# Kernel optimization log

Measured on AMD Instinct MI355X. Metric: run time of the kernel, lower is better.

The kernel has to match this reference:

```python
import jax, jax.numpy as jnp
import numpy as np

B = 16
NS = 1024   # coarse points per cloud
NT = 4096   # fine (skip) points per cloud
CIN = 256
CSK = 64
H = 256
K = 3


def setup_inputs() -> dict:
    key = jax.random.key(0)
    ks = jax.random.split(key, 8)
    x = jax.random.normal(ks[0], (B * NS, CIN), dtype=jnp.float32)
    pos = jax.random.normal(ks[1], (B * NS, 3), dtype=jnp.float32)
    x_skip = jax.random.normal(ks[2], (B * NT, CSK), dtype=jnp.float32)
    pos_skip = jax.random.normal(ks[3], (B * NT, 3), dtype=jnp.float32)
    batch = jnp.repeat(jnp.arange(B, dtype=jnp.int64), NS)
    batch_skip = jnp.repeat(jnp.arange(B, dtype=jnp.int64), NT)
    W1 = jax.random.normal(ks[4], (CIN + CSK, H), dtype=jnp.float32) / np.sqrt(CIN + CSK)
    b1 = jnp.zeros((H,), dtype=jnp.float32)
    W2 = jax.random.normal(ks[5], (H, H), dtype=jnp.float32) / np.sqrt(H)
    b2 = jnp.zeros((H,), dtype=jnp.float32)
    return {"x": x, "pos": pos, "x_skip": x_skip, "pos_skip": pos_skip,
            "W1": W1, "b1": b1, "W2": W2, "b2": b2,
            "batch": batch, "batch_skip": batch_skip}


def _knn_interpolate(x, pos, pos_skip):
    # x: [B*NS, C], pos: [B*NS, 3], pos_skip: [B*NT, 3]; equal-size clouds,
    # batch ids are contiguous so per-cloud kNN == reshape to [B, N, .]
    xb = x.reshape(B, NS, -1)
    pb = pos.reshape(B, NS, 3)
    qb = pos_skip.reshape(B, NT, 3)
    # squared distances [B, NT, NS]
    d2 = jnp.sum((qb[:, :, None, :] - pb[:, None, :, :]) ** 2, axis=-1)
    neg_d2k, idx = jax.lax.top_k(-d2, K)            # [B, NT, K]
    w = 1.0 / jnp.maximum(-neg_d2k, 1e-16)          # inverse squared distance
    feats = jax.vmap(lambda xc, ic: xc[ic])(xb, idx)  # [B, NT, K, C]
    y = jnp.sum(feats * w[..., None], axis=2) / jnp.sum(w, axis=2, keepdims=True)
    return y.reshape(B * NT, -1)


def reference(x, pos, x_skip, pos_skip, W1, b1, W2, b2, batch, batch_skip):
    xi = _knn_interpolate(x, pos, pos_skip)          # [B*NT, CIN]
    h = jnp.concatenate([xi, x_skip], axis=1)        # [B*NT, CIN+CSK]
    h = jax.nn.relu(h @ W1 + b1)
    h = jax.nn.relu(h @ W2 + b2)
    return (h, pos_skip, batch_skip)
```

## Files before the change

### kernel.cpp

```cpp
#include <hip/hip_runtime.h>
#include <hip/hip_bf16.h>

#define BB   16
#define NS   1024
#define NT   4096
#define CIN  256
#define CSK  64
#define HD   256
#define K1   (CIN + CSK)
#define MTOT (BB * NT)

typedef __attribute__((ext_vector_type(4))) float f32x4;
typedef __attribute__((ext_vector_type(8))) __bf16 bf16x8;
typedef __attribute__((ext_vector_type(4))) unsigned short ushort4v;

#define W1F_OFF 0u
#define W2F_OFF 163840u

static __device__ __forceinline__ unsigned short f2bf(float f) {
    union { float f; unsigned int u; } v; v.f = f;
    unsigned int r = (v.u + 0x7FFFu + ((v.u >> 16) & 1u)) >> 16;
    return (unsigned short)r;
}
static __device__ __forceinline__ unsigned short f2bf_hw(float f) {
    union { __bf16 b; unsigned short u; } v; v.b = (__bf16)f;
    return v.u;
}

#define PREP_B1 (K1 * HD / 256)
#define PREP_B2 (HD * HD / 256)
#define PREP_B3 ((MTOT * 3) / 256)
__global__ __launch_bounds__(256) void prep_kernel(
    const float* __restrict__ W1, const float* __restrict__ W2,
    const float* __restrict__ pos_skip,
    unsigned short* __restrict__ W1f, unsigned short* __restrict__ W2f,
    float* __restrict__ out)
{
    const int b = blockIdx.x;
    if (b < PREP_B1 + PREP_B2) {
        const bool is1 = b < PREP_B1;
        const int id = (is1 ? b : b - PREP_B1) * 256 + threadIdx.x;
        const int j    = id & 7;
        const int lane = (id >> 3) & 63;
        const int n    = (id >> 9) & 15;
        const int kblk = id >> 13;
        const int k   = kblk * 32 + (lane >> 4) * 8 + j;
        const int col = n * 16 + (lane & 15);
        if (is1) W1f[id] = f2bf(W1[(size_t)k * HD + col]);
        else     W2f[id] = f2bf(W2[(size_t)k * HD + col]);
    } else {
        const int i = (b - PREP_B1 - PREP_B2) * 256 + threadIdx.x;
        const size_t o1 = (size_t)MTOT * HD;
        out[o1 + i] = pos_skip[i];
        if (i < MTOT) out[o1 + (size_t)MTOT * 3 + i] = (float)(i >> 12);
    }
}

__global__ __launch_bounds__(256, 4) void fp_fused_kernel(
    const float* __restrict__ x, const float* __restrict__ x_skip,
    const float* __restrict__ pos, const float* __restrict__ pos_skip,
    const unsigned short* __restrict__ W1f, const unsigned short* __restrict__ W2f,
    const float* __restrict__ b1, const float* __restrict__ b2,
    float* __restrict__ out)
{
    __shared__ __align__(16) unsigned short ldsA[10 * 4 * 512];

    const int tid = threadIdx.x;
    const int w = tid >> 6, lane = tid & 63;
    const int l15 = lane & 15, lk = lane >> 4;

    const int bid   = blockIdx.x;
    const int xcd   = bid & 7;
    const int j     = bid >> 3;
    const int cloud = xcd + 8 * (j >> 6);
    const int bm    = cloud * 64 + (j & 63);

    int   myi0, myi1, myi2;
    float myw0, myw1, myw2;
    {
        float4* sp = (float4*)ldsA;
        const float* pc = pos + (size_t)cloud * NS * 3;
        for (int i = tid; i < NS; i += 256)
            sp[i] = make_float4(pc[i * 3 + 0], pc[i * 3 + 1], pc[i * 3 + 2], 0.f);
        __syncthreads();

        const int p  = tid & 3;
        const int rg = bm * 64 + (tid >> 2);
        const float qx = pos_skip[rg * 3 + 0];
        const float qy = pos_skip[rg * 3 + 1];
        const float qz = pos_skip[rg * 3 + 2];

        double b0 = 1e300, b1k = 1e300, b2k = 1e300;
        double si = (double)p;
        #pragma unroll 4
        for (int i = 0; i < NS / 4; ++i) {
            const int s = i * 4 + p;
            float4 c = sp[s];
            float dx = qx - c.x, dy = qy - c.y, dz = qz - c.z;
            float d = dx * dx + dy * dy + dz * dz;
            double key = fma((double)__float_as_uint(d), 1024.0, si);
            si += 4.0;
            double nb0 = fmin(b0, key);
            double nb1 = fmax(b0, fmin(b1k, key));
            double nb2 = fmax(b1k, fmin(b2k, key));
            b0 = nb0; b1k = nb1; b2k = nb2;
        }
        #pragma unroll
        for (int m = 1; m <= 2; m <<= 1) {
            double o0 = __shfl_xor(b0, m, 64);
            double o1 = __shfl_xor(b1k, m, 64);
            double o2 = __shfl_xor(b2k, m, 64);
            double nb0, nb1, nb2;
            nb0 = fmin(b0, o0); nb1 = fmax(b0, fmin(b1k, o0)); nb2 = fmax(b1k, fmin(b2k, o0));
            b0 = nb0; b1k = nb1; b2k = nb2;
            nb0 = fmin(b0, o1); nb1 = fmax(b0, fmin(b1k, o1)); nb2 = fmax(b1k, fmin(b2k, o1));
            b0 = nb0; b1k = nb1; b2k = nb2;
            nb0 = fmin(b0, o2); nb1 = fmax(b0, fmin(b1k, o2)); nb2 = fmax(b1k, fmin(b2k, o2));
            b0 = nb0; b1k = nb1; b2k = nb2;
        }
        unsigned long long k0 = (unsigned long long)b0;
        unsigned long long k1 = (unsigned long long)b1k;
        unsigned long long k2 = (unsigned long long)b2k;
        myi0 = (int)(k0 & 1023ull);
        myi1 = (int)(k1 & 1023ull);
        myi2 = (int)(k2 & 1023ull);
        float d0 = __uint_as_float((unsigned int)(k0 >> 10));
        float d1 = __uint_as_float((unsigned int)(k1 >> 10));
        float d2 = __uint_as_float((unsigned int)(k2 >> 10));
        float w0 = 1.f / fmaxf(d0, 1e-16f);
        float w1 = 1.f / fmaxf(d1, 1e-16f);
        float w2 = 1.f / fmaxf(d2, 1e-16f);
        float inv = 1.f / (w0 + w1 + w2);
        myw0 = w0 * inv; myw1 = w1 * inv; myw2 = w2 * inv;
        __syncthreads();
    }

    {
        const int cb  = cloud * NS;
        const int kbm = lane >> 3;
        const int lkm = (lane >> 1) & 3;
        const int em  = lane & 1;
        const int kbs = 8 + (lane >> 5);
        const int lks = (lane >> 3) & 3;
        const int jjs = lane & 7;
        #pragma unroll
        for (int r16 = 0; r16 < 16; ++r16) {
            const int src = r16 * 4;
            const int i0 = cb + __shfl(myi0, src, 64);
            const int i1 = cb + __shfl(myi1, src, 64);
            const int i2 = cb + __shfl(myi2, src, 64);
            const float w0 = __shfl(myw0, src, 64);
            const float w1 = __shfl(myw1, src, 64);
            const float w2 = __shfl(myw2, src, 64);
            const int row = w * 16 + r16;
            const int rg  = bm * 64 + row;
            f32x4 a = *(const f32x4*)(x + (size_t)i0 * CIN + lane * 4);
            f32x4 b = *(const f32x4*)(x + (size_t)i1 * CIN + lane * 4);
            f32x4 c = *(const f32x4*)(x + (size_t)i2 * CIN + lane * 4);
            float s = x_skip[(size_t)rg * CSK + lane];
            f32x4 r = a * w0 + b * w1 + c * w2;
            int H = ((kbm * 4 + w) * 64 + (r16 + 16 * lkm)) * 8 + 4 * em;
            H ^= (kbm & 7) << 3;
            ushort4v o4 = { f2bf_hw(r[0]), f2bf_hw(r[1]), f2bf_hw(r[2]), f2bf_hw(r[3]) };
            *(ushort4v*)&ldsA[H] = o4;
            int H2 = ((kbs * 4 + w) * 64 + (r16 + 16 * lks)) * 8 + jjs;
            H2 ^= (kbs & 7) << 3;
            ldsA[H2] = f2bf_hw(s);
        }
    }
    __syncthreads();

    const unsigned short* w1p = W1f + (w * 4) * 512 + lane * 8;
    const unsigned short* w2p = W2f + (w * 4) * 512 + lane * 8;

    f32x4 acc[4][4];
    #pragma unroll
    for (int mf = 0; mf < 4; ++mf)
        #pragma unroll
        for (int nf = 0; nf < 4; ++nf)
            acc[mf][nf] = f32x4{0.f, 0.f, 0.f, 0.f};

    {
        bf16x8 bc[4], bn[4];
        #pragma unroll
        for (int nf = 0; nf < 4; ++nf)
            bc[nf] = *(const bf16x8*)(w1p + nf * 512);
        #pragma unroll
        for (int kb = 0; kb < 10; ++kb) {
            if (kb < 9) {
                #pragma unroll
                for (int nf = 0; nf < 4; ++nf)
                    bn[nf] = *(const bf16x8*)(w1p + (size_t)(kb + 1) * 8192 + nf * 512);
            }
            bf16x8 a[4];
            #pragma unroll
            for (int mf = 0; mf < 4; ++mf) {
                int aoff = ((kb * 4 + mf) * 64 + lane) * 8;
                aoff ^= (kb & 7) << 3;
                a[mf] = *(const bf16x8*)&ldsA[aoff];
            }
            #pragma unroll
            for (int mf = 0; mf < 4; ++mf)
                #pragma unroll
                for (int nf = 0; nf < 4; ++nf)
                    acc[mf][nf] = __builtin_amdgcn_mfma_f32_16x16x32_bf16(
                        a[mf], bc[nf], acc[mf][nf], 0, 0, 0);
            #pragma unroll
            for (int nf = 0; nf < 4; ++nf) bc[nf] = bn[nf];
        }
    }
    __syncthreads();

    #pragma unroll
    for (int nf = 0; nf < 4; ++nf) {
        const int col = w * 64 + nf * 16 + l15;
        const float bv = b1[col];
        const int kb2   = 2 * w + (nf >> 1);
        const int lane2 = lk * 4 + 16 * ((nf & 1) * 2 + (l15 >> 3));
        #pragma unroll
        for (int mf = 0; mf < 4; ++mf) {
            #pragma unroll
            for (int r = 0; r < 4; ++r) {
                float v = fmaxf(acc[mf][nf][r] + bv, 0.f);
                ldsA[((kb2 * 4 + mf) * 64 + lane2 + r) * 8 + (l15 & 7)] = f2bf_hw(v);
            }
        }
    }
    __syncthreads();

    f32x4 acc2[4][4];
    #pragma unroll
    for (int mf = 0; mf < 4; ++mf)
        #pragma unroll
        for (int nf = 0; nf < 4; ++nf)
            acc2[mf][nf] = f32x4{0.f, 0.f, 0.f, 0.f};

    {
        bf16x8 bc[4], bn[4];
        #pragma unroll
        for (int nf = 0; nf < 4; ++nf)
            bc[nf] = *(const bf16x8*)(w2p + nf * 512);
        #pragma unroll
        for (int kb = 0; kb < 8; ++kb) {
            if (kb < 7) {
                #pragma unroll
                for (int nf = 0; nf < 4; ++nf)
                    bn[nf] = *(const bf16x8*)(w2p + (size_t)(kb + 1) * 8192 + nf * 512);
            }
            bf16x8 a[4];
            #pragma unroll
            for (int mf = 0; mf < 4; ++mf)
                a[mf] = *(const bf16x8*)&ldsA[((kb * 4 + mf) * 64 + lane) * 8];
            #pragma unroll
            for (int mf = 0; mf < 4; ++mf)
                #pragma unroll
                for (int nf = 0; nf < 4; ++nf)
                    acc2[mf][nf] = __builtin_amdgcn_mfma_f32_16x16x32_bf16(
                        a[mf], bc[nf], acc2[mf][nf], 0, 0, 0);
            #pragma unroll
            for (int nf = 0; nf < 4; ++nf) bc[nf] = bn[nf];
        }
    }

    const int rbase = bm * 64 + lk * 4;
    const int cbase = w * 64 + l15;
    #pragma unroll
    for (int nf = 0; nf < 4; ++nf) {
        const int col = cbase + nf * 16;
        const float bv = b2[col];
        #pragma unroll
        for (int mf = 0; mf < 4; ++mf) {
            #pragma unroll
            for (int r = 0; r < 4; ++r) {
                float v = fmaxf(acc2[mf][nf][r] + bv, 0.f);
                out[(size_t)(rbase + mf * 16 + r) * HD + col] = v;
            }
        }
    }
}

extern "C" void kernel_launch(void* const* d_in, const int* in_sizes, int n_in,
                              void* d_out, int out_size, void* d_ws, size_t ws_size,
                              hipStream_t stream)
{
    const float* x        = (const float*)d_in[0];
    const float* pos      = (const float*)d_in[1];
    const float* x_skip   = (const float*)d_in[2];
    const float* pos_skip = (const float*)d_in[3];
    const float* W1       = (const float*)d_in[4];
    const float* b1       = (const float*)d_in[5];
    const float* W2       = (const float*)d_in[6];
    const float* b2       = (const float*)d_in[7];
    float* out = (float*)d_out;

    char* ws = (char*)d_ws;
    unsigned short* W1f  = (unsigned short*)(ws + W1F_OFF);
    unsigned short* W2f  = (unsigned short*)(ws + W2F_OFF);

    prep_kernel<<<PREP_B1 + PREP_B2 + PREP_B3, 256, 0, stream>>>(
        W1, W2, pos_skip, W1f, W2f, out);
    fp_fused_kernel<<<MTOT / 64, 256, 0, stream>>>(
        x, x_skip, pos, pos_skip, W1f, W2f, b1, b2, out);
}
```

Before: 62.84 us.

## Replace packed-double top-3 kNN with float/index pairwise insertion network

The per-query top-3 search now tracks float distances and unsigned indices separately instead of packing them into double keys with fp64 min/max. Candidates are processed two at a time: the pair is sorted first and then merged into the running top-3 with a short compare network. The cross-lane reduction uses explicit tie-breaking on index. Separately, the first W1 fragment loads are issued at kernel start so their latency overlaps the kNN phase, at the cost of extra live registers during the search.

```diff
diff --git a/kernel.cpp b/kernel.cpp
--- a/kernel.cpp
+++ b/kernel.cpp
@@ -75,6 +75,13 @@
     const int cloud = xcd + 8 * (j >> 6);
     const int bm    = cloud * 64 + (j & 63);
 
+    const unsigned short* w1p = W1f + (w * 4) * 512 + lane * 8;
+    const unsigned short* w2p = W2f + (w * 4) * 512 + lane * 8;
+    bf16x8 bpre[4];
+    #pragma unroll
+    for (int nf = 0; nf < 4; ++nf)
+        bpre[nf] = *(const bf16x8*)(w1p + nf * 512);
+
     int   myi0, myi1, myi2;
     float myw0, myw1, myw2;
     {
@@ -90,46 +97,61 @@
         const float qy = pos_skip[rg * 3 + 1];
         const float qz = pos_skip[rg * 3 + 2];
 
-        double b0 = 1e300, b1k = 1e300, b2k = 1e300;
-        double si = (double)p;
-        #pragma unroll 4
-        for (int i = 0; i < NS / 4; ++i) {
-            const int s = i * 4 + p;
-            float4 c = sp[s];
-            float dx = qx - c.x, dy = qy - c.y, dz = qz - c.z;
-            float d = dx * dx + dy * dy + dz * dz;
-            double key = fma((double)__float_as_uint(d), 1024.0, si);
-            si += 4.0;
-            double nb0 = fmin(b0, key);
-            double nb1 = fmax(b0, fmin(b1k, key));
-            double nb2 = fmax(b1k, fmin(b2k, key));
-            b0 = nb0; b1k = nb1; b2k = nb2;
+        float d0 = 1e30f, d1k = 1e30f, d2k = 1e30f;
+        unsigned i0 = 0, i1 = 0, i2 = 0;
+        #pragma unroll 2
+        for (int ii = 0; ii < NS / 8; ++ii) {
+            const int slo = ii * 8 + p;
+            const int shi = slo + 4;
+            float4 ca = sp[slo];
+            float4 cb = sp[shi];
+            float dxa = qx - ca.x, dya = qy - ca.y, dza = qz - ca.z;
+            float da = dxa * dxa + dya * dya + dza * dza;
+            float dxb = qx - cb.x, dyb = qy - cb.y, dzb = qz - cb.z;
+            float db = dxb * dxb + dyb * dyb + dzb * dzb;
+            bool cs = db < da;
+            float    dlo = cs ? db : da,           dhi = cs ? da : db;
+            unsigned ilo = cs ? (unsigned)shi : (unsigned)slo;
+            unsigned ihi = cs ? (unsigned)slo : (unsigned)shi;
+            bool c0 = dlo < d0;
+            float    x0d = c0 ? dlo : d0,  x1d = c0 ? d0 : dlo;
+            unsigned x0i = c0 ? ilo : i0,  x1i = c0 ? i0 : ilo;
+            bool cy = dhi < d1k;
+            float    y0d = cy ? dhi : d1k;
+            unsigned y0i = cy ? ihi : i1;
+            bool cr = y0d < x1d;
+            float    r1d = cr ? y0d : x1d, td = cr ? x1d : y0d;
+            unsigned r1i = cr ? y0i : x1i; unsigned ti = cr ? x1i : y0i;
+            bool c2 = td < d2k;
+            float    r2d = c2 ? td : d2k;
+            unsigned r2i = c2 ? ti : i2;
+            d0 = x0d; i0 = x0i; d1k = r1d; i1 = r1i; d2k = r2d; i2 = r2i;
         }
         #pragma unroll
         for (int m = 1; m <= 2; m <<= 1) {
-            double o0 = __shfl_xor(b0, m, 64);
-            double o1 = __shfl_xor(b1k, m, 64);
-            double o2 = __shfl_xor(b2k, m, 64);
-            double nb0, nb1, nb2;
-            nb0 = fmin(b0, o0); nb1 = fmax(b0, fmin(b1k, o0)); nb2 = fmax(b1k, fmin(b2k, o0));
-            b0 = nb0; b1k = nb1; b2k = nb2;
-            nb0 = fmin(b0, o1); nb1 = fmax(b0, fmin(b1k, o1)); nb2 = fmax(b1k, fmin(b2k, o1));
-            b0 = nb0; b1k = nb1; b2k = nb2;
-            nb0 = fmin(b0, o2); nb1 = fmax(b0, fmin(b1k, o2)); nb2 = fmax(b1k, fmin(b2k, o2));
-            b0 = nb0; b1k = nb1; b2k = nb2;
-        }
-        unsigned long long k0 = (unsigned long long)b0;
-        unsigned long long k1 = (unsigned long long)b1k;
-        unsigned long long k2 = (unsigned long long)b2k;
-        myi0 = (int)(k0 & 1023ull);
-        myi1 = (int)(k1 & 1023ull);
-        myi2 = (int)(k2 & 1023ull);
-        float d0 = __uint_as_float((unsigned int)(k0 >> 10));
-        float d1 = __uint_as_float((unsigned int)(k1 >> 10));
-        float d2 = __uint_as_float((unsigned int)(k2 >> 10));
+            float    od0 = __shfl_xor(d0, m, 64);
+            float    od1 = __shfl_xor(d1k, m, 64);
+            float    od2 = __shfl_xor(d2k, m, 64);
+            unsigned oi0 = (unsigned)__shfl_xor((int)i0, m, 64);
+            unsigned oi1 = (unsigned)__shfl_xor((int)i1, m, 64);
+            unsigned oi2 = (unsigned)__shfl_xor((int)i2, m, 64);
+            float od[3] = { od0, od1, od2 };
+            unsigned oi[3] = { oi0, oi1, oi2 };
+            #pragma unroll
+            for (int e = 0; e < 3; ++e) {
+                float dd = od[e]; unsigned ss = oi[e];
+                bool lt0 = (dd < d0)  || (dd == d0  && ss < i0);
+                bool lt1 = (dd < d1k) || (dd == d1k && ss < i1);
+                bool lt2 = (dd < d2k) || (dd == d2k && ss < i2);
+                d2k = lt1 ? d1k : (lt2 ? dd : d2k);  i2 = lt1 ? i1 : (lt2 ? ss : i2);
+                d1k = lt0 ? d0  : (lt1 ? dd : d1k);  i1 = lt0 ? i0 : (lt1 ? ss : i1);
+                d0  = lt0 ? dd  : d0;                i0 = lt0 ? ss : i0;
+            }
+        }
+        myi0 = (int)i0; myi1 = (int)i1; myi2 = (int)i2;
         float w0 = 1.f / fmaxf(d0, 1e-16f);
-        float w1 = 1.f / fmaxf(d1, 1e-16f);
-        float w2 = 1.f / fmaxf(d2, 1e-16f);
+        float w1 = 1.f / fmaxf(d1k, 1e-16f);
+        float w2 = 1.f / fmaxf(d2k, 1e-16f);
         float inv = 1.f / (w0 + w1 + w2);
         myw0 = w0 * inv; myw1 = w1 * inv; myw2 = w2 * inv;
         __syncthreads();
@@ -170,9 +192,6 @@
     }
     __syncthreads();
 
-    const unsigned short* w1p = W1f + (w * 4) * 512 + lane * 8;
-    const unsigned short* w2p = W2f + (w * 4) * 512 + lane * 8;
-
     f32x4 acc[4][4];
     #pragma unroll
     for (int mf = 0; mf < 4; ++mf)
@@ -183,8 +202,7 @@
     {
         bf16x8 bc[4], bn[4];
         #pragma unroll
-        for (int nf = 0; nf < 4; ++nf)
-            bc[nf] = *(const bf16x8*)(w1p + nf * 512);
+        for (int nf = 0; nf < 4; ++nf) bc[nf] = bpre[nf];
         #pragma unroll
         for (int kb = 0; kb < 10; ++kb) {
             if (kb < 9) {
```

Result: slower. 67.79 us (+7.9%).

## Process two row tiles per block and overlap next tile's kNN with MLP MFMAs

Applied to the files above, without the earlier changes.

Each block now handles two 64-row tiles of the same cloud. The kNN search for the second tile is split into chunks and interleaved with the MFMA loops of the first tile's two GEMMs, so VALU distance work can hide behind matrix-core work. The coarse positions get their own LDS array and are loaded once per two tiles. The grid is halved and launch bounds drop to 2 blocks per SM, which lowers occupancy and raises register pressure, and the GEMM k-loops are no longer fully unrolled.

```diff
diff --git a/kernel.cpp b/kernel.cpp
--- a/kernel.cpp
+++ b/kernel.cpp
@@ -56,71 +56,85 @@
     }
 }
 
-__global__ __launch_bounds__(256, 4) void fp_fused_kernel(
+__global__ __launch_bounds__(256, 2) void fp_fused_kernel(
     const float* __restrict__ x, const float* __restrict__ x_skip,
     const float* __restrict__ pos, const float* __restrict__ pos_skip,
     const unsigned short* __restrict__ W1f, const unsigned short* __restrict__ W2f,
     const float* __restrict__ b1, const float* __restrict__ b2,
     float* __restrict__ out)
 {
+    __shared__ float4 sp[NS];
     __shared__ __align__(16) unsigned short ldsA[10 * 4 * 512];
 
     const int tid = threadIdx.x;
     const int w = tid >> 6, lane = tid & 63;
     const int l15 = lane & 15, lk = lane >> 4;
+    const int p    = tid & 3;
+    const int qloc = tid >> 2;
 
     const int bid   = blockIdx.x;
     const int xcd   = bid & 7;
     const int j     = bid >> 3;
-    const int cloud = xcd + 8 * (j >> 6);
-    const int bm    = cloud * 64 + (j & 63);
-
-    int   myi0, myi1, myi2;
-    float myw0, myw1, myw2;
+    const int cloud = xcd + 8 * (j >> 5);
+    const int j2    = j & 31;
+    const int bm0   = cloud * 64 + j2 * 2;
+    const int bm1   = bm0 + 1;
+
+    const unsigned short* w1p = W1f + (w * 4) * 512 + lane * 8;
+    const unsigned short* w2p = W2f + (w * 4) * 512 + lane * 8;
+
     {
-        float4* sp = (float4*)ldsA;
         const float* pc = pos + (size_t)cloud * NS * 3;
         for (int i = tid; i < NS; i += 256)
             sp[i] = make_float4(pc[i * 3 + 0], pc[i * 3 + 1], pc[i * 3 + 2], 0.f);
-        __syncthreads();
-
-        const int p  = tid & 3;
-        const int rg = bm * 64 + (tid >> 2);
-        const float qx = pos_skip[rg * 3 + 0];
-        const float qy = pos_skip[rg * 3 + 1];
-        const float qz = pos_skip[rg * 3 + 2];
-
-        double b0 = 1e300, b1k = 1e300, b2k = 1e300;
-        double si = (double)p;
+    }
+    __syncthreads();
+
+    double kb0_, kb1_, kb2_, ksi_;
+    float  kqx, kqy, kqz;
+    int    myi0, myi1, myi2;
+    float  myw0, myw1, myw2;
+
+    auto knn_init = [&](int bm) {
+        const int rg = bm * 64 + qloc;
+        kqx = pos_skip[rg * 3 + 0];
+        kqy = pos_skip[rg * 3 + 1];
+        kqz = pos_skip[rg * 3 + 2];
+        kb0_ = 1e300; kb1_ = 1e300; kb2_ = 1e300;
+        ksi_ = (double)p;
+    };
+    auto knn_chunk = [&](int start, int cnt) {
         #pragma unroll 4
-        for (int i = 0; i < NS / 4; ++i) {
-            const int s = i * 4 + p;
+        for (int t = 0; t < cnt; ++t) {
+            const int s = (start + t) * 4 + p;
             float4 c = sp[s];
-            float dx = qx - c.x, dy = qy - c.y, dz = qz - c.z;
+            float dx = kqx - c.x, dy = kqy - c.y, dz = kqz - c.z;
             float d = dx * dx + dy * dy + dz * dz;
-            double key = fma((double)__float_as_uint(d), 1024.0, si);
-            si += 4.0;
-            double nb0 = fmin(b0, key);
-            double nb1 = fmax(b0, fmin(b1k, key));
-            double nb2 = fmax(b1k, fmin(b2k, key));
-            b0 = nb0; b1k = nb1; b2k = nb2;
-        }
+            double key = fma((double)__float_as_uint(d), 1024.0, ksi_);
+            ksi_ += 4.0;
+            double nb0 = fmin(kb0_, key);
+            double nb1 = fmax(kb0_, fmin(kb1_, key));
+            double nb2 = fmax(kb1_, fmin(kb2_, key));
+            kb0_ = nb0; kb1_ = nb1; kb2_ = nb2;
+        }
+    };
+    auto knn_finish = [&]() {
         #pragma unroll
         for (int m = 1; m <= 2; m <<= 1) {
-            double o0 = __shfl_xor(b0, m, 64);
-            double o1 = __shfl_xor(b1k, m, 64);
-            double o2 = __shfl_xor(b2k, m, 64);
+            double o0 = __shfl_xor(kb0_, m, 64);
+            double o1 = __shfl_xor(kb1_, m, 64);
+            double o2 = __shfl_xor(kb2_, m, 64);
             double nb0, nb1, nb2;
-            nb0 = fmin(b0, o0); nb1 = fmax(b0, fmin(b1k, o0)); nb2 = fmax(b1k, fmin(b2k, o0));
-            b0 = nb0; b1k = nb1; b2k = nb2;
-            nb0 = fmin(b0, o1); nb1 = fmax(b0, fmin(b1k, o1)); nb2 = fmax(b1k, fmin(b2k, o1));
-            b0 = nb0; b1k = nb1; b2k = nb2;
-            nb0 = fmin(b0, o2); nb1 = fmax(b0, fmin(b1k, o2)); nb2 = fmax(b1k, fmin(b2k, o2));
-            b0 = nb0; b1k = nb1; b2k = nb2;
-        }
-        unsigned long long k0 = (unsigned long long)b0;
-        unsigned long long k1 = (unsigned long long)b1k;
-        unsigned long long k2 = (unsigned long long)b2k;
+            nb0 = fmin(kb0_, o0); nb1 = fmax(kb0_, fmin(kb1_, o0)); nb2 = fmax(kb1_, fmin(kb2_, o0));
+            kb0_ = nb0; kb1_ = nb1; kb2_ = nb2;
+            nb0 = fmin(kb0_, o1); nb1 = fmax(kb0_, fmin(kb1_, o1)); nb2 = fmax(kb1_, fmin(kb2_, o1));
+            kb0_ = nb0; kb1_ = nb1; kb2_ = nb2;
+            nb0 = fmin(kb0_, o2); nb1 = fmax(kb0_, fmin(kb1_, o2)); nb2 = fmax(kb1_, fmin(kb2_, o2));
+            kb0_ = nb0; kb1_ = nb1; kb2_ = nb2;
+        }
+        unsigned long long k0 = (unsigned long long)kb0_;
+        unsigned long long k1 = (unsigned long long)kb1_;
+        unsigned long long k2 = (unsigned long long)kb2_;
         myi0 = (int)(k0 & 1023ull);
         myi1 = (int)(k1 & 1023ull);
         myi2 = (int)(k2 & 1023ull);
@@ -132,10 +146,9 @@
         float w2 = 1.f / fmaxf(d2, 1e-16f);
         float inv = 1.f / (w0 + w1 + w2);
         myw0 = w0 * inv; myw1 = w1 * inv; myw2 = w2 * inv;
-        __syncthreads();
-    }
-
-    {
+    };
+
+    auto gather = [&](int bm) {
         const int cb  = cloud * NS;
         const int kbm = lane >> 3;
         const int lkm = (lane >> 1) & 3;
@@ -167,116 +180,127 @@
             H2 ^= (kbs & 7) << 3;
             ldsA[H2] = f2bf_hw(s);
         }
-    }
+    };
+
+    auto run_group = [&](int bm, bool doknn) {
+        f32x4 acc[4][4];
+        #pragma unroll
+        for (int mf = 0; mf < 4; ++mf)
+            #pragma unroll
+            for (int nf = 0; nf < 4; ++nf)
+                acc[mf][nf] = f32x4{0.f, 0.f, 0.f, 0.f};
+        {
+            bf16x8 bc[4], bn[4];
+            #pragma unroll
+            for (int nf = 0; nf < 4; ++nf)
+                bc[nf] = *(const bf16x8*)(w1p + nf * 512);
+            for (int kb = 0; kb < 10; ++kb) {
+                if (kb < 9) {
+                    #pragma unroll
+                    for (int nf = 0; nf < 4; ++nf)
+                        bn[nf] = *(const bf16x8*)(w1p + (size_t)(kb + 1) * 8192 + nf * 512);
+                }
+                bf16x8 a[4];
+                #pragma unroll
+                for (int mf = 0; mf < 4; ++mf) {
+                    int aoff = ((kb * 4 + mf) * 64 + lane) * 8;
+                    aoff ^= (kb & 7) << 3;
+                    a[mf] = *(const bf16x8*)&ldsA[aoff];
+                }
+                #pragma unroll
+                for (int mf = 0; mf < 4; ++mf)
+                    #pragma unroll
+                    for (int nf = 0; nf < 4; ++nf)
+                        acc[mf][nf] = __builtin_amdgcn_mfma_f32_16x16x32_bf16(
+                            a[mf], bc[nf], acc[mf][nf], 0, 0, 0);
+                if (doknn) knn_chunk(kb * 16, 16);
+                #pragma unroll
+                for (int nf = 0; nf < 4; ++nf) bc[nf] = bn[nf];
+            }
+        }
+        __syncthreads();
+
+        #pragma unroll
+        for (int nf = 0; nf < 4; ++nf) {
+            const int col = w * 64 + nf * 16 + l15;
+            const float bv = b1[col];
+            const int kb2   = 2 * w + (nf >> 1);
+            const int lane2 = lk * 4 + 16 * ((nf & 1) * 2 + (l15 >> 3));
+            #pragma unroll
+            for (int mf = 0; mf < 4; ++mf) {
+                #pragma unroll
+                for (int r = 0; r < 4; ++r) {
+                    float v = fmaxf(acc[mf][nf][r] + bv, 0.f);
+                    ldsA[((kb2 * 4 + mf) * 64 + lane2 + r) * 8 + (l15 & 7)] = f2bf_hw(v);
+                }
+            }
+        }
+        __syncthreads();
+
+        f32x4 acc2[4][4];
+        #pragma unroll
+        for (int mf = 0; mf < 4; ++mf)
+            #pragma unroll
+            for (int nf = 0; nf < 4; ++nf)
+                acc2[mf][nf] = f32x4{0.f, 0.f, 0.f, 0.f};
+        {
+            bf16x8 bc[4], bn[4];
+            #pragma unroll
+            for (int nf = 0; nf < 4; ++nf)
+                bc[nf] = *(const bf16x8*)(w2p + nf * 512);
+            for (int kb = 0; kb < 8; ++kb) {
+                if (kb < 7) {
+                    #pragma unroll
+                    for (int nf = 0; nf < 4; ++nf)
+                        bn[nf] = *(const bf16x8*)(w2p + (size_t)(kb + 1) * 8192 + nf * 512);
+                }
+                bf16x8 a[4];
+                #pragma unroll
+                for (int mf = 0; mf < 4; ++mf)
+                    a[mf] = *(const bf16x8*)&ldsA[((kb * 4 + mf) * 64 + lane) * 8];
+                #pragma unroll
+                for (int mf = 0; mf < 4; ++mf)
+                    #pragma unroll
+                    for (int nf = 0; nf < 4; ++nf)
+                        acc2[mf][nf] = __builtin_amdgcn_mfma_f32_16x16x32_bf16(
+                            a[mf], bc[nf], acc2[mf][nf], 0, 0, 0);
+                if (doknn) knn_chunk(160 + kb * 12, 12);
+                #pragma unroll
+                for (int nf = 0; nf < 4; ++nf) bc[nf] = bn[nf];
+            }
+        }
+        const int rbase = bm * 64 + lk * 4;
+        const int cbase = w * 64 + l15;
+        #pragma unroll
+        for (int nf = 0; nf < 4; ++nf) {
+            const int col = cbase + nf * 16;
+            const float bv = b2[col];
+            #pragma unroll
+            for (int mf = 0; mf < 4; ++mf) {
+                #pragma unroll
+                for (int r = 0; r < 4; ++r) {
+                    float v = fmaxf(acc2[mf][nf][r] + bv, 0.f);
+                    out[(size_t)(rbase + mf * 16 + r) * HD + col] = v;
+                }
+            }
+        }
+    };
+
+    knn_init(bm0);
+    knn_chunk(0, 256);
+    knn_finish();
+    gather(bm0);
     __syncthreads();
 
-    const unsigned short* w1p = W1f + (w * 4) * 512 + lane * 8;
-    const unsigned short* w2p = W2f + (w * 4) * 512 + lane * 8;
-
-    f32x4 acc[4][4];
-    #pragma unroll
-    for (int mf = 0; mf < 4; ++mf)
-        #pragma unroll
-        for (int nf = 0; nf < 4; ++nf)
-            acc[mf][nf] = f32x4{0.f, 0.f, 0.f, 0.f};
-
-    {
-        bf16x8 bc[4], bn[4];
-        #pragma unroll
-        for (int nf = 0; nf < 4; ++nf)
-            bc[nf] = *(const bf16x8*)(w1p + nf * 512);
-        #pragma unroll
-        for (int kb = 0; kb < 10; ++kb) {
-            if (kb < 9) {
-                #pragma unroll
-                for (int nf = 0; nf < 4; ++nf)
-                    bn[nf] = *(const bf16x8*)(w1p + (size_t)(kb + 1) * 8192 + nf * 512);
-            }
-            bf16x8 a[4];
-            #pragma unroll
-            for (int mf = 0; mf < 4; ++mf) {
-                int aoff = ((kb * 4 + mf) * 64 + lane) * 8;
-                aoff ^= (kb & 7) << 3;
-                a[mf] = *(const bf16x8*)&ldsA[aoff];
-            }
-            #pragma unroll
-            for (int mf = 0; mf < 4; ++mf)
-                #pragma unroll
-                for (int nf = 0; nf < 4; ++nf)
-                    acc[mf][nf] = __builtin_amdgcn_mfma_f32_16x16x32_bf16(
-                        a[mf], bc[nf], acc[mf][nf], 0, 0, 0);
-            #pragma unroll
-            for (int nf = 0; nf < 4; ++nf) bc[nf] = bn[nf];
-        }
-    }
+    knn_init(bm1);
+    run_group(bm0, true);
     __syncthreads();
 
-    #pragma unroll
-    for (int nf = 0; nf < 4; ++nf) {
-        const int col = w * 64 + nf * 16 + l15;
-        const float bv = b1[col];
-        const int kb2   = 2 * w + (nf >> 1);
-        const int lane2 = lk * 4 + 16 * ((nf & 1) * 2 + (l15 >> 3));
-        #pragma unroll
-        for (int mf = 0; mf < 4; ++mf) {
-            #pragma unroll
-            for (int r = 0; r < 4; ++r) {
-                float v = fmaxf(acc[mf][nf][r] + bv, 0.f);
-                ldsA[((kb2 * 4 + mf) * 64 + lane2 + r) * 8 + (l15 & 7)] = f2bf_hw(v);
-            }
-        }
-    }
+    knn_finish();
+    gather(bm1);
     __syncthreads();
 
-    f32x4 acc2[4][4];
-    #pragma unroll
-    for (int mf = 0; mf < 4; ++mf)
-        #pragma unroll
-        for (int nf = 0; nf < 4; ++nf)
-            acc2[mf][nf] = f32x4{0.f, 0.f, 0.f, 0.f};
-
-    {
-        bf16x8 bc[4], bn[4];
-        #pragma unroll
-        for (int nf = 0; nf < 4; ++nf)
-            bc[nf] = *(const bf16x8*)(w2p + nf * 512);
-        #pragma unroll
-        for (int kb = 0; kb < 8; ++kb) {
-            if (kb < 7) {
-                #pragma unroll
-                for (int nf = 0; nf < 4; ++nf)
-                    bn[nf] = *(const bf16x8*)(w2p + (size_t)(kb + 1) * 8192 + nf * 512);
-            }
-            bf16x8 a[4];
-            #pragma unroll
-            for (int mf = 0; mf < 4; ++mf)
-                a[mf] = *(const bf16x8*)&ldsA[((kb * 4 + mf) * 64 + lane) * 8];
-            #pragma unroll
-            for (int mf = 0; mf < 4; ++mf)
-                #pragma unroll
-                for (int nf = 0; nf < 4; ++nf)
-                    acc2[mf][nf] = __builtin_amdgcn_mfma_f32_16x16x32_bf16(
-                        a[mf], bc[nf], acc2[mf][nf], 0, 0, 0);
-            #pragma unroll
-            for (int nf = 0; nf < 4; ++nf) bc[nf] = bn[nf];
-        }
-    }
-
-    const int rbase = bm * 64 + lk * 4;
-    const int cbase = w * 64 + l15;
-    #pragma unroll
-    for (int nf = 0; nf < 4; ++nf) {
-        const int col = cbase + nf * 16;
-        const float bv = b2[col];
-        #pragma unroll
-        for (int mf = 0; mf < 4; ++mf) {
-            #pragma unroll
-            for (int r = 0; r < 4; ++r) {
-                float v = fmaxf(acc2[mf][nf][r] + bv, 0.f);
-                out[(size_t)(rbase + mf * 16 + r) * HD + col] = v;
-            }
-        }
-    }
+    run_group(bm1, false);
 }
 
 extern "C" void kernel_launch(void* const* d_in, const int* in_sizes, int n_in,
@@ -299,6 +323,6 @@
 
     prep_kernel<<<PREP_B1 + PREP_B2 + PREP_B3, 256, 0, stream>>>(
         W1, W2, pos_skip, W1f, W2f, out);
-    fp_fused_kernel<<<MTOT / 64, 256, 0, stream>>>(
+    fp_fused_kernel<<<MTOT / 128, 256, 0, stream>>>(
         x, x_skip, pos, pos_skip, W1f, W2f, b1, b2, out);
 }
```

Measured after the change: 98.21 us. 1.56x slower.
